# Kernel optimization log

Measured on AMD Instinct MI355X. Metric: run time of the kernel, lower is better.

Reference implementation:

```python
import jax, jax.numpy as jnp
import numpy as np

EPS = 1e-7  # K.epsilon()
NUM_CAPSULE = 32
DIM_CAPSULE = 16
ROUTINGS = 3


def squash(x, axis=-1):
    # NOTE: this repo's squash is pure L2 normalization (no |s|^2/(1+|s|^2) factor)
    s2 = jnp.sum(jnp.square(x), axis=axis, keepdims=True)
    return x / jnp.sqrt(s2 + EPS)


def setup_inputs() -> dict:
    key = jax.random.key(0)
    k1, k2 = jax.random.split(key)
    B, L, D_IN = 32, 2048, 64
    u_vecs = jax.random.normal(k1, (B, L, D_IN), dtype=jnp.float32)
    # glorot-ish scale for the capsule kernel
    W = jax.random.normal(k2, (1, D_IN, NUM_CAPSULE * DIM_CAPSULE), dtype=jnp.float32) * 0.05
    return {"u_vecs": u_vecs, "W": W}


def reference(u_vecs, W):
    B, L, _ = u_vecs.shape
    # K.conv1d with kernel size 1 == pointwise matmul
    u_hat = jnp.einsum('bli,io->blo', u_vecs, W[0])
    u_hat = u_hat.reshape(B, L, NUM_CAPSULE, DIM_CAPSULE)
    u_hat = jnp.transpose(u_hat, (0, 2, 1, 3))  # [B, nc, L, dc]

    b = jnp.zeros((B, NUM_CAPSULE, L), dtype=u_hat.dtype)
    outputs = None
    for i in range(ROUTINGS):
        # softmax over the num_capsule axis (axis=1), per the permute dance in the source
        c = jax.nn.softmax(b, axis=1)  # [B, nc, L]
        outputs = squash(jnp.einsum('bnl,bnld->bnd', c, u_hat))  # [B, nc, dc]
        if i < ROUTINGS - 1:
            b = jnp.einsum('bnd,bnld->bnl', outputs, u_hat)  # overwrite, not accumulate
    return outputs
```

## Files before the change

### kernel.cpp

```cpp
#include <hip/hip_runtime.h>

#define NC 32
#define DC 16
#define LSEQ 2048

__global__ __launch_bounds__(256) void k_sum_u(const float* __restrict__ u,
                                               float* __restrict__ v0p) {
    int b  = blockIdx.x >> 3;
    int l0 = (blockIdx.x & 7) * 256;
    int q  = threadIdx.x & 15;
    int r  = threadIdx.x >> 4;
    const float4* u4 = (const float4*)u;
    float4 acc = {0.f, 0.f, 0.f, 0.f};
#pragma unroll
    for (int j = 0; j < 16; ++j) {
        int l = l0 + r + 16 * j;
        float4 x = u4[(b * LSEQ + l) * 16 + q];
        acc.x += x.x; acc.y += x.y; acc.z += x.z; acc.w += x.w;
    }
    __shared__ float red[16][64];
    red[r][q * 4 + 0] = acc.x;
    red[r][q * 4 + 1] = acc.y;
    red[r][q * 4 + 2] = acc.z;
    red[r][q * 4 + 3] = acc.w;
    __syncthreads();
    if (threadIdx.x < 64) {
        float s = 0.f;
#pragma unroll
        for (int rr = 0; rr < 16; ++rr) s += red[rr][threadIdx.x];
        v0p[blockIdx.x * 64 + threadIdx.x] = s;
    }
}

template <bool BCAST, bool FINAL>
__global__ __launch_bounds__(64) void k_caps(const float* __restrict__ v,
                                             const float* __restrict__ W,
                                             float* __restrict__ wtil,
                                             float* __restrict__ out,
                                             float vscale) {
    int b  = blockIdx.x >> 3;
    int ng = blockIdx.x & 7;
    int t  = threadIdx.x;
    __shared__ float vS[4][72];
    __shared__ float oS[4][16];
    if (BCAST) {
        float s = 0.f;
#pragma unroll
        for (int ch = 0; ch < 8; ++ch) s += v[(b * 8 + ch) * 64 + t];
        s *= vscale;
#pragma unroll
        for (int n4 = 0; n4 < 4; ++n4) vS[n4][t] = s;
    } else {
        int row = t >> 4, col4 = t & 15;
        const float4* v4 = (const float4*)v;
        float4 a = {0.f, 0.f, 0.f, 0.f};
#pragma unroll
        for (int ch = 0; ch < 16; ++ch) {
            float4 x = v4[(b * 16 + ch) * 512 + (ng * 4 + row) * 16 + col4];
            a.x += x.x; a.y += x.y; a.z += x.z; a.w += x.w;
        }
        ((float4*)&vS[row][0])[col4] = a;
    }
    __syncthreads();
    int n4 = t >> 4, d = t & 15;
    int n  = ng * 4 + n4;
    const float* vrow = &vS[n4][0];
    float s = 0.f;
#pragma unroll
    for (int i = 0; i < 64; ++i)
        s = fmaf(vrow[i], W[i * (NC * DC) + n * DC + d], s);
    float s2 = s * s;
#pragma unroll
    for (int off = 8; off >= 1; off >>= 1) s2 += __shfl_xor(s2, off, 16);
    float o = s / sqrtf(s2 + 1e-7f);
    if (FINAL) {
        out[b * (NC * DC) + n * DC + d] = o;
    } else {
        oS[n4][d] = o;
        __syncthreads();
        int i4 = t & 15;
        float4 wv;
        float* wvp = (float*)&wv;
#pragma unroll
        for (int k = 0; k < 4; ++k) {
            int i = i4 * 4 + k;
            float acc = 0.f;
#pragma unroll
            for (int dd = 0; dd < 16; ++dd)
                acc = fmaf(W[i * (NC * DC) + n * DC + dd], oS[n4][dd], acc);
            wvp[k] = acc;
        }
        ((float4*)wtil)[(b * (NC * 64) + n * 64 + i4 * 4) >> 2] = wv;
    }
}

__global__ __launch_bounds__(128) void k_route(const float* __restrict__ u,
                                               const float* __restrict__ wtil,
                                               float* __restrict__ vpart) {
    int b    = blockIdx.x >> 4;
    int ch   = blockIdx.x & 15;
    int l0   = ch * 128;
    int t    = threadIdx.x;
    int w    = t >> 6;
    int lane = t & 63;
    int lr   = lane & 7;
    int lc   = lane >> 3;
    int dr   = lane & 7;
    int nc   = lane >> 3;

    __shared__ float uS[128 * 68];
    __shared__ float wS[32 * 68];
    __shared__ float cS[2 * 2304];
    float4* uS4 = (float4*)uS;
    float4* wS4 = (float4*)wS;
    float*  cw  = cS + w * 2304;
    float4* cw4 = (float4*)cw;

    const float4* ug = (const float4*)(u + (b * LSEQ + l0) * 64);
#pragma unroll
    for (int r = 0; r < 16; ++r) {
        int idx = t + 128 * r;
        uS4[(idx >> 4) * 17 + (idx & 15)] = ug[idx];
    }
    const float4* wg = (const float4*)(wtil + b * (NC * 64));
#pragma unroll
    for (int r = 0; r < 4; ++r) {
        int idx = t + 128 * r;
        wS4[(idx >> 4) * 17 + (idx & 15)] = wg[idx];
    }
    __syncthreads();

    float acc[8][4];
#pragma unroll
    for (int i = 0; i < 8; ++i)
#pragma unroll
        for (int j = 0; j < 4; ++j) acc[i][j] = 0.f;
    int arow = w * 64 + lr;
#pragma unroll 4
    for (int k4 = 0; k4 < 16; ++k4) {
        float4 wf[4];
#pragma unroll
        for (int j = 0; j < 4; ++j) wf[j] = wS4[(lc * 4 + j) * 17 + k4];
#pragma unroll
        for (int i = 0; i < 8; ++i) {
            float4 a = uS4[(arow + 8 * i) * 17 + k4];
#pragma unroll
            for (int j = 0; j < 4; ++j) {
                acc[i][j] = fmaf(a.x, wf[j].x, acc[i][j]);
                acc[i][j] = fmaf(a.y, wf[j].y, acc[i][j]);
                acc[i][j] = fmaf(a.z, wf[j].z, acc[i][j]);
                acc[i][j] = fmaf(a.w, wf[j].w, acc[i][j]);
            }
        }
    }

#pragma unroll
    for (int i = 0; i < 8; ++i) {
        float m = fmaxf(fmaxf(acc[i][0], acc[i][1]), fmaxf(acc[i][2], acc[i][3]));
        m = fmaxf(m, __shfl_xor(m, 8));
        m = fmaxf(m, __shfl_xor(m, 16));
        m = fmaxf(m, __shfl_xor(m, 32));
        float e0 = __expf(acc[i][0] - m), e1 = __expf(acc[i][1] - m);
        float e2 = __expf(acc[i][2] - m), e3 = __expf(acc[i][3] - m);
        float ss = e0 + e1 + e2 + e3;
        ss += __shfl_xor(ss, 8);
        ss += __shfl_xor(ss, 16);
        ss += __shfl_xor(ss, 32);
        float inv = 1.f / ss;
        float4 cvv = {e0 * inv, e1 * inv, e2 * inv, e3 * inv};
        cw4[(lr + 8 * i) * 9 + lc] = cvv;
    }
    __syncthreads();

    float vacc[4][8];
#pragma unroll
    for (int j = 0; j < 4; ++j)
#pragma unroll
        for (int k = 0; k < 8; ++k) vacc[j][k] = 0.f;
#pragma unroll 8
    for (int lrel = 0; lrel < 64; ++lrel) {
        float4 cv = cw4[lrel * 9 + nc];
        const float4* ur = uS4 + (w * 64 + lrel) * 17 + dr * 2;
        float4 u0 = ur[0], u1 = ur[1];
        float* cp = (float*)&cv;
#pragma unroll
        for (int j = 0; j < 4; ++j) {
            float c = cp[j];
            vacc[j][0] = fmaf(c, u0.x, vacc[j][0]);
            vacc[j][1] = fmaf(c, u0.y, vacc[j][1]);
            vacc[j][2] = fmaf(c, u0.z, vacc[j][2]);
            vacc[j][3] = fmaf(c, u0.w, vacc[j][3]);
            vacc[j][4] = fmaf(c, u1.x, vacc[j][4]);
            vacc[j][5] = fmaf(c, u1.y, vacc[j][5]);
            vacc[j][6] = fmaf(c, u1.z, vacc[j][6]);
            vacc[j][7] = fmaf(c, u1.w, vacc[j][7]);
        }
    }

#pragma unroll
    for (int j = 0; j < 4; ++j) {
        float* rp = cw + (nc * 4 + j) * 64 + dr * 8;
        float4 r0 = {vacc[j][0], vacc[j][1], vacc[j][2], vacc[j][3]};
        float4 r1 = {vacc[j][4], vacc[j][5], vacc[j][6], vacc[j][7]};
        ((float4*)rp)[0] = r0;
        ((float4*)rp)[1] = r1;
    }
    __syncthreads();
    float4* cS4 = (float4*)cS;
    float4* vp4 = (float4*)(vpart + blockIdx.x * 2048);
#pragma unroll
    for (int s = 0; s < 4; ++s) {
        int idx4 = t + 128 * s;
        float4 a = cS4[idx4];
        float4 c2 = cS4[576 + idx4];
        float4 o = {a.x + c2.x, a.y + c2.y, a.z + c2.z, a.w + c2.w};
        vp4[idx4] = o;
    }
}

extern "C" void kernel_launch(void* const* d_in, const int* in_sizes, int n_in,
                              void* d_out, int out_size, void* d_ws, size_t ws_size,
                              hipStream_t stream) {
    const float* u = (const float*)d_in[0];
    const float* W = (const float*)d_in[1];
    float* out = (float*)d_out;
    float* ws  = (float*)d_ws;
    float* v0p   = ws;
    float* wt    = ws + 16384;
    float* vpart = ws + 16384 + 65536;

    k_sum_u<<<256, 256, 0, stream>>>(u, v0p);
    k_caps<true, false><<<256, 64, 0, stream>>>(v0p, W, wt, nullptr, 1.0f / 32.0f);
    k_route<<<512, 128, 0, stream>>>(u, wt, vpart);
    k_caps<false, false><<<256, 64, 0, stream>>>(vpart, W, wt, nullptr, 1.0f);
    k_route<<<512, 128, 0, stream>>>(u, wt, vpart);
    k_caps<false, true><<<256, 64, 0, stream>>>(vpart, W, nullptr, out, 1.0f);
}
```

Before: 107.6 us.

## Fuse capsule squash/W-projection into routing kernels via last-block atomic counters

Merges the per-batch capsule computation (v reduction, W projection, squash, and the W·o projection for the next iteration) into the tail of the preceding sum or routing kernel. The last block per batch is detected with an atomic counter and a threadfence, which replaces the separate k_caps launches. This cuts six launches to three plus a memset and regroups block indices so that all chunks of a batch run close together. In exchange, the serial tail work lands on a single 128-thread block per batch and adds atomic and fence overhead.

```diff
diff --git a/kernel.cpp b/kernel.cpp
--- a/kernel.cpp
+++ b/kernel.cpp
@@ -4,125 +4,126 @@
 #define DC 16
 #define LSEQ 2048
 
-__global__ __launch_bounds__(256) void k_sum_u(const float* __restrict__ u,
-                                               float* __restrict__ v0p) {
-    int b  = blockIdx.x >> 3;
-    int l0 = (blockIdx.x & 7) * 256;
-    int q  = threadIdx.x & 15;
-    int r  = threadIdx.x >> 4;
-    const float4* u4 = (const float4*)u;
-    float4 acc = {0.f, 0.f, 0.f, 0.f};
-#pragma unroll
-    for (int j = 0; j < 16; ++j) {
-        int l = l0 + r + 16 * j;
-        float4 x = u4[(b * LSEQ + l) * 16 + q];
-        acc.x += x.x; acc.y += x.y; acc.z += x.z; acc.w += x.w;
-    }
-    __shared__ float red[16][64];
-    red[r][q * 4 + 0] = acc.x;
-    red[r][q * 4 + 1] = acc.y;
-    red[r][q * 4 + 2] = acc.z;
-    red[r][q * 4 + 3] = acc.w;
-    __syncthreads();
-    if (threadIdx.x < 64) {
+
+
+__global__ __launch_bounds__(128) void k_sum_caps0(const float* __restrict__ u,
+                                                   const float* __restrict__ W,
+                                                   float* __restrict__ v0p,
+                                                   float* __restrict__ wtil,
+                                                   int* __restrict__ ctr) {
+    const int rid = blockIdx.x;
+    const int b   = (rid & 7) + ((rid >> 7) << 3);
+    const int j   = (rid >> 3) & 15;
+    const int gb  = b * 16 + j;
+    const int t   = threadIdx.x;
+
+    __shared__ float red[512];
+    __shared__ float vS[64];
+    __shared__ float oS[512];
+    __shared__ int amLast;
+
+    const float4* ug = (const float4*)(u + (b * LSEQ + j * 128) * 64);
+    float4 a = {0.f, 0.f, 0.f, 0.f};
+#pragma unroll
+    for (int r = 0; r < 16; ++r) {
+        float4 x = ug[t + 128 * r];
+        a.x += x.x; a.y += x.y; a.z += x.z; a.w += x.w;
+    }
+    ((float4*)red)[t] = a;
+    __syncthreads();
+    if (t < 64) {
         float s = 0.f;
 #pragma unroll
-        for (int rr = 0; rr < 16; ++rr) s += red[rr][threadIdx.x];
-        v0p[blockIdx.x * 64 + threadIdx.x] = s;
+        for (int g = 0; g < 8; ++g) s += red[t + 64 * g];
+        v0p[gb * 64 + t] = s;
+    }
+    __syncthreads();
+    if (t == 0) {
+        __threadfence();
+        int prev = atomicAdd(&ctr[b * 32 + 0], 1);
+        amLast = (prev == 15);
+    }
+    __syncthreads();
+    if (!amLast) return;
+    __threadfence();
+
+    if (t < 64) {
+        float s = 0.f;
+#pragma unroll
+        for (int ch = 0; ch < 16; ++ch) s += v0p[(b * 16 + ch) * 64 + t];
+        vS[t] = s * (1.f / 32.f);
+    }
+    __syncthreads();
+
+    const int n = t >> 2, d4 = t & 3;
+    const float4* W4 = (const float4*)W;
+    float4 s4 = {0.f, 0.f, 0.f, 0.f};
+#pragma unroll
+    for (int i = 0; i < 64; ++i) {
+        float vi = vS[i];
+        float4 wv = W4[i * 128 + n * 4 + d4];
+        s4.x = fmaf(vi, wv.x, s4.x);
+        s4.y = fmaf(vi, wv.y, s4.y);
+        s4.z = fmaf(vi, wv.z, s4.z);
+        s4.w = fmaf(vi, wv.w, s4.w);
+    }
+    float s2 = s4.x * s4.x + s4.y * s4.y + s4.z * s4.z + s4.w * s4.w;
+    s2 += __shfl_xor(s2, 1);
+    s2 += __shfl_xor(s2, 2);
+    float inv = 1.f / sqrtf(s2 + 1e-7f);
+    float4 o4 = {s4.x * inv, s4.y * inv, s4.z * inv, s4.w * inv};
+    ((float4*)oS)[t] = o4;
+    __syncthreads();
+
+    const float4* oS4 = (const float4*)oS;
+#pragma unroll
+    for (int rep = 0; rep < 16; ++rep) {
+        int idx = t + 128 * rep;
+        int nn = idx >> 6, ii = idx & 63;
+        float acc = 0.f;
+#pragma unroll
+        for (int q = 0; q < 4; ++q) {
+            float4 wv = W4[ii * 128 + nn * 4 + q];
+            float4 ov = oS4[nn * 4 + q];
+            acc += wv.x * ov.x + wv.y * ov.y + wv.z * ov.z + wv.w * ov.w;
+        }
+        wtil[b * (NC * 64) + idx] = acc;
     }
 }
 
-template <bool BCAST, bool FINAL>
-__global__ __launch_bounds__(64) void k_caps(const float* __restrict__ v,
-                                             const float* __restrict__ W,
-                                             float* __restrict__ wtil,
-                                             float* __restrict__ out,
-                                             float vscale) {
-    int b  = blockIdx.x >> 3;
-    int ng = blockIdx.x & 7;
-    int t  = threadIdx.x;
-    __shared__ float vS[4][72];
-    __shared__ float oS[4][16];
-    if (BCAST) {
-        float s = 0.f;
-#pragma unroll
-        for (int ch = 0; ch < 8; ++ch) s += v[(b * 8 + ch) * 64 + t];
-        s *= vscale;
-#pragma unroll
-        for (int n4 = 0; n4 < 4; ++n4) vS[n4][t] = s;
-    } else {
-        int row = t >> 4, col4 = t & 15;
-        const float4* v4 = (const float4*)v;
-        float4 a = {0.f, 0.f, 0.f, 0.f};
-#pragma unroll
-        for (int ch = 0; ch < 16; ++ch) {
-            float4 x = v4[(b * 16 + ch) * 512 + (ng * 4 + row) * 16 + col4];
-            a.x += x.x; a.y += x.y; a.z += x.z; a.w += x.w;
-        }
-        ((float4*)&vS[row][0])[col4] = a;
-    }
-    __syncthreads();
-    int n4 = t >> 4, d = t & 15;
-    int n  = ng * 4 + n4;
-    const float* vrow = &vS[n4][0];
-    float s = 0.f;
-#pragma unroll
-    for (int i = 0; i < 64; ++i)
-        s = fmaf(vrow[i], W[i * (NC * DC) + n * DC + d], s);
-    float s2 = s * s;
-#pragma unroll
-    for (int off = 8; off >= 1; off >>= 1) s2 += __shfl_xor(s2, off, 16);
-    float o = s / sqrtf(s2 + 1e-7f);
-    if (FINAL) {
-        out[b * (NC * DC) + n * DC + d] = o;
-    } else {
-        oS[n4][d] = o;
-        __syncthreads();
-        int i4 = t & 15;
-        float4 wv;
-        float* wvp = (float*)&wv;
-#pragma unroll
-        for (int k = 0; k < 4; ++k) {
-            int i = i4 * 4 + k;
-            float acc = 0.f;
-#pragma unroll
-            for (int dd = 0; dd < 16; ++dd)
-                acc = fmaf(W[i * (NC * DC) + n * DC + dd], oS[n4][dd], acc);
-            wvp[k] = acc;
-        }
-        ((float4*)wtil)[(b * (NC * 64) + n * 64 + i4 * 4) >> 2] = wv;
-    }
-}
-
-__global__ __launch_bounds__(128) void k_route(const float* __restrict__ u,
-                                               const float* __restrict__ wtil,
-                                               float* __restrict__ vpart) {
-    int b    = blockIdx.x >> 4;
-    int ch   = blockIdx.x & 15;
-    int l0   = ch * 128;
-    int t    = threadIdx.x;
-    int w    = t >> 6;
-    int lane = t & 63;
-    int lr   = lane & 7;
-    int lc   = lane >> 3;
-    int dr   = lane & 7;
-    int nc   = lane >> 3;
+template <int PH, bool FINAL>
+__global__ __launch_bounds__(128) void k_route_caps(const float* __restrict__ u,
+                                                    const float* __restrict__ W,
+                                                    const float* __restrict__ wtil_in,
+                                                    float* __restrict__ wtil_out,
+                                                    float* __restrict__ out,
+                                                    float* __restrict__ vpart,
+                                                    int* __restrict__ ctr) {
+    const int rid  = blockIdx.x;
+    const int b    = (rid & 7) + ((rid >> 7) << 3);
+    const int j    = (rid >> 3) & 15;
+    const int gb   = b * 16 + j;
+    const int t    = threadIdx.x;
+    const int w    = t >> 6;
+    const int lane = t & 63;
 
     __shared__ float uS[128 * 68];
     __shared__ float wS[32 * 68];
     __shared__ float cS[2 * 2304];
+    __shared__ int amLast;
     float4* uS4 = (float4*)uS;
     float4* wS4 = (float4*)wS;
+    float4* cS4 = (float4*)cS;
     float*  cw  = cS + w * 2304;
     float4* cw4 = (float4*)cw;
 
-    const float4* ug = (const float4*)(u + (b * LSEQ + l0) * 64);
+    const float4* ug = (const float4*)(u + (b * LSEQ + j * 128) * 64);
 #pragma unroll
     for (int r = 0; r < 16; ++r) {
         int idx = t + 128 * r;
         uS4[(idx >> 4) * 17 + (idx & 15)] = ug[idx];
     }
-    const float4* wg = (const float4*)(wtil + b * (NC * 64));
+    const float4* wg = (const float4*)(wtil_in + b * (NC * 64));
 #pragma unroll
     for (int r = 0; r < 4; ++r) {
         int idx = t + 128 * r;
@@ -130,26 +131,27 @@
     }
     __syncthreads();
 
+    const int lr = lane & 7, lc = lane >> 3;
     float acc[8][4];
 #pragma unroll
     for (int i = 0; i < 8; ++i)
 #pragma unroll
-        for (int j = 0; j < 4; ++j) acc[i][j] = 0.f;
-    int arow = w * 64 + lr;
+        for (int jj = 0; jj < 4; ++jj) acc[i][jj] = 0.f;
+    const int arow = w * 64 + lr;
 #pragma unroll 4
     for (int k4 = 0; k4 < 16; ++k4) {
         float4 wf[4];
 #pragma unroll
-        for (int j = 0; j < 4; ++j) wf[j] = wS4[(lc * 4 + j) * 17 + k4];
+        for (int jj = 0; jj < 4; ++jj) wf[jj] = wS4[(lc * 4 + jj) * 17 + k4];
 #pragma unroll
         for (int i = 0; i < 8; ++i) {
-            float4 a = uS4[(arow + 8 * i) * 17 + k4];
-#pragma unroll
-            for (int j = 0; j < 4; ++j) {
-                acc[i][j] = fmaf(a.x, wf[j].x, acc[i][j]);
-                acc[i][j] = fmaf(a.y, wf[j].y, acc[i][j]);
-                acc[i][j] = fmaf(a.z, wf[j].z, acc[i][j]);
-                acc[i][j] = fmaf(a.w, wf[j].w, acc[i][j]);
+            float4 av = uS4[(arow + 8 * i) * 17 + k4];
+#pragma unroll
+            for (int jj = 0; jj < 4; ++jj) {
+                acc[i][jj] = fmaf(av.x, wf[jj].x, acc[i][jj]);
+                acc[i][jj] = fmaf(av.y, wf[jj].y, acc[i][jj]);
+                acc[i][jj] = fmaf(av.z, wf[jj].z, acc[i][jj]);
+                acc[i][jj] = fmaf(av.w, wf[jj].w, acc[i][jj]);
             }
         }
     }
@@ -172,49 +174,113 @@
     }
     __syncthreads();
 
+    const int dr = lane & 7, ng = lane >> 3;
     float vacc[4][8];
 #pragma unroll
-    for (int j = 0; j < 4; ++j)
-#pragma unroll
-        for (int k = 0; k < 8; ++k) vacc[j][k] = 0.f;
+    for (int jj = 0; jj < 4; ++jj)
+#pragma unroll
+        for (int k = 0; k < 8; ++k) vacc[jj][k] = 0.f;
 #pragma unroll 8
     for (int lrel = 0; lrel < 64; ++lrel) {
-        float4 cv = cw4[lrel * 9 + nc];
+        float4 cv = cw4[lrel * 9 + ng];
         const float4* ur = uS4 + (w * 64 + lrel) * 17 + dr * 2;
         float4 u0 = ur[0], u1 = ur[1];
         float* cp = (float*)&cv;
 #pragma unroll
-        for (int j = 0; j < 4; ++j) {
-            float c = cp[j];
-            vacc[j][0] = fmaf(c, u0.x, vacc[j][0]);
-            vacc[j][1] = fmaf(c, u0.y, vacc[j][1]);
-            vacc[j][2] = fmaf(c, u0.z, vacc[j][2]);
-            vacc[j][3] = fmaf(c, u0.w, vacc[j][3]);
-            vacc[j][4] = fmaf(c, u1.x, vacc[j][4]);
-            vacc[j][5] = fmaf(c, u1.y, vacc[j][5]);
-            vacc[j][6] = fmaf(c, u1.z, vacc[j][6]);
-            vacc[j][7] = fmaf(c, u1.w, vacc[j][7]);
-        }
-    }
-
-#pragma unroll
-    for (int j = 0; j < 4; ++j) {
-        float* rp = cw + (nc * 4 + j) * 64 + dr * 8;
-        float4 r0 = {vacc[j][0], vacc[j][1], vacc[j][2], vacc[j][3]};
-        float4 r1 = {vacc[j][4], vacc[j][5], vacc[j][6], vacc[j][7]};
+        for (int jj = 0; jj < 4; ++jj) {
+            float c = cp[jj];
+            vacc[jj][0] = fmaf(c, u0.x, vacc[jj][0]);
+            vacc[jj][1] = fmaf(c, u0.y, vacc[jj][1]);
+            vacc[jj][2] = fmaf(c, u0.z, vacc[jj][2]);
+            vacc[jj][3] = fmaf(c, u0.w, vacc[jj][3]);
+            vacc[jj][4] = fmaf(c, u1.x, vacc[jj][4]);
+            vacc[jj][5] = fmaf(c, u1.y, vacc[jj][5]);
+            vacc[jj][6] = fmaf(c, u1.z, vacc[jj][6]);
+            vacc[jj][7] = fmaf(c, u1.w, vacc[jj][7]);
+        }
+    }
+#pragma unroll
+    for (int jj = 0; jj < 4; ++jj) {
+        float* rp = cw + (ng * 4 + jj) * 64 + dr * 8;
+        float4 r0 = {vacc[jj][0], vacc[jj][1], vacc[jj][2], vacc[jj][3]};
+        float4 r1 = {vacc[jj][4], vacc[jj][5], vacc[jj][6], vacc[jj][7]};
         ((float4*)rp)[0] = r0;
         ((float4*)rp)[1] = r1;
     }
     __syncthreads();
-    float4* cS4 = (float4*)cS;
-    float4* vp4 = (float4*)(vpart + blockIdx.x * 2048);
-#pragma unroll
-    for (int s = 0; s < 4; ++s) {
-        int idx4 = t + 128 * s;
-        float4 a = cS4[idx4];
-        float4 c2 = cS4[576 + idx4];
-        float4 o = {a.x + c2.x, a.y + c2.y, a.z + c2.z, a.w + c2.w};
+    float4* vp4 = (float4*)(vpart + gb * 2048);
+#pragma unroll
+    for (int sft = 0; sft < 4; ++sft) {
+        int idx4 = t + 128 * sft;
+        float4 x = cS4[idx4];
+        float4 y = cS4[576 + idx4];
+        float4 o = {x.x + y.x, x.y + y.y, x.z + y.z, x.w + y.w};
         vp4[idx4] = o;
+    }
+    __syncthreads();
+
+    if (t == 0) {
+        __threadfence();
+        int prev = atomicAdd(&ctr[b * 32 + PH], 1);
+        amLast = (prev == 15);
+    }
+    __syncthreads();
+    if (!amLast) return;
+    __threadfence();
+
+    const float4* vpb = (const float4*)(vpart + b * 16 * 2048);
+#pragma unroll
+    for (int rep = 0; rep < 4; ++rep) {
+        int idx4 = t + 128 * rep;
+        float4 s = {0.f, 0.f, 0.f, 0.f};
+#pragma unroll
+        for (int ch = 0; ch < 16; ++ch) {
+            float4 x = vpb[ch * 512 + idx4];
+            s.x += x.x; s.y += x.y; s.z += x.z; s.w += x.w;
+        }
+        cS4[(idx4 >> 4) * 17 + (idx4 & 15)] = s;
+    }
+    __syncthreads();
+
+    const int n = t >> 2, d4 = t & 3;
+    const float4* W4 = (const float4*)W;
+    const float* vrow = &cS[n * 68];
+    float4 s4 = {0.f, 0.f, 0.f, 0.f};
+#pragma unroll
+    for (int i = 0; i < 64; ++i) {
+        float vi = vrow[i];
+        float4 wv = W4[i * 128 + n * 4 + d4];
+        s4.x = fmaf(vi, wv.x, s4.x);
+        s4.y = fmaf(vi, wv.y, s4.y);
+        s4.z = fmaf(vi, wv.z, s4.z);
+        s4.w = fmaf(vi, wv.w, s4.w);
+    }
+    float s2 = s4.x * s4.x + s4.y * s4.y + s4.z * s4.z + s4.w * s4.w;
+    s2 += __shfl_xor(s2, 1);
+    s2 += __shfl_xor(s2, 2);
+    float inv = 1.f / sqrtf(s2 + 1e-7f);
+    float4 o4 = {s4.x * inv, s4.y * inv, s4.z * inv, s4.w * inv};
+
+    if (FINAL) {
+        ((float4*)out)[b * 128 + t] = o4;
+        return;
+    }
+    float* oS = cS + 2304;
+    ((float4*)oS)[t] = o4;
+    __syncthreads();
+    const float4* oS4 = (const float4*)oS;
+#pragma unroll
+    for (int rep = 0; rep < 16; ++rep) {
+        int idx = t + 128 * rep;
+        int nn = idx >> 6, ii = idx & 63;
+        float a2 = 0.f;
+#pragma unroll
+        for (int q = 0; q < 4; ++q) {
+            float4 wv = W4[ii * 128 + nn * 4 + q];
+            float4 ov = oS4[nn * 4 + q];
+            a2 += wv.x * ov.x + wv.y * ov.y + wv.z * ov.z + wv.w * ov.w;
+        }
+        wtil_out[b * (NC * 64) + idx] = a2;
     }
 }
 
@@ -225,14 +291,14 @@
     const float* W = (const float*)d_in[1];
     float* out = (float*)d_out;
     float* ws  = (float*)d_ws;
-    float* v0p   = ws;
-    float* wt    = ws + 16384;
-    float* vpart = ws + 16384 + 65536;
-
-    k_sum_u<<<256, 256, 0, stream>>>(u, v0p);
-    k_caps<true, false><<<256, 64, 0, stream>>>(v0p, W, wt, nullptr, 1.0f / 32.0f);
-    k_route<<<512, 128, 0, stream>>>(u, wt, vpart);
-    k_caps<false, false><<<256, 64, 0, stream>>>(vpart, W, wt, nullptr, 1.0f);
-    k_route<<<512, 128, 0, stream>>>(u, wt, vpart);
-    k_caps<false, true><<<256, 64, 0, stream>>>(vpart, W, nullptr, out, 1.0f);
+    int*   ctr   = (int*)ws;
+    float* v0p   = ws + 1024;
+    float* wt    = ws + 1024 + 16384;
+    float* vpart = ws + 1024 + 16384 + 65536;
+
+    hipMemsetAsync(ctr, 0, 32 * 32 * sizeof(int), stream);
+
+    k_sum_caps0<<<512, 128, 0, stream>>>(u, W, v0p, wt, ctr);
+    k_route_caps<1, false><<<512, 128, 0, stream>>>(u, W, wt, wt, nullptr, vpart, ctr);
+    k_route_caps<2, true ><<<512, 128, 0, stream>>>(u, W, wt, nullptr, out, vpart, ctr);
 }
```

After: 155.2 us. 1.44x slower.

## Fuse capsule head into routing kernel and reduce partials with atomics

Applied to the files above, without the earlier changes.

The per-iteration capsule projection and squash step, which computes the W-transformed output vectors, now runs redundantly at the start of every routing block instead of in its own kernel. Partial sums over the sequence are accumulated with global atomicAdd into zeroed workspace instead of being written out and reduced by the next kernel. Routing blocks now use 512 threads over 128 rows, each wave handling 16 rows. Together this cuts the launch count from six kernels to four plus a memset, at the cost of recomputing the head in every block and of atomic contention with nondeterministic summation order.

```diff
diff --git a/kernel.cpp b/kernel.cpp
--- a/kernel.cpp
+++ b/kernel.cpp
@@ -4,158 +4,142 @@
 #define DC 16
 #define LSEQ 2048
 
-__global__ __launch_bounds__(256) void k_sum_u(const float* __restrict__ u,
-                                               float* __restrict__ v0p) {
-    int b  = blockIdx.x >> 3;
-    int l0 = (blockIdx.x & 7) * 256;
-    int q  = threadIdx.x & 15;
-    int r  = threadIdx.x >> 4;
-    const float4* u4 = (const float4*)u;
-    float4 acc = {0.f, 0.f, 0.f, 0.f};
-#pragma unroll
-    for (int j = 0; j < 16; ++j) {
-        int l = l0 + r + 16 * j;
-        float4 x = u4[(b * LSEQ + l) * 16 + q];
-        acc.x += x.x; acc.y += x.y; acc.z += x.z; acc.w += x.w;
+__global__ __launch_bounds__(256) void k_sum(const float* __restrict__ u,
+                                             float* __restrict__ v0) {
+    const int b = blockIdx.x >> 4, j = blockIdx.x & 15;
+    const int t = threadIdx.x;
+    const int q = t & 15, r = t >> 4;
+    const float4* ug = (const float4*)(u + (b * LSEQ + j * 128) * 64);
+    float4 a = {0.f, 0.f, 0.f, 0.f};
+#pragma unroll
+    for (int g = 0; g < 8; ++g) {
+        float4 x = ug[(r + 16 * g) * 16 + q];
+        a.x += x.x; a.y += x.y; a.z += x.z; a.w += x.w;
     }
     __shared__ float red[16][64];
-    red[r][q * 4 + 0] = acc.x;
-    red[r][q * 4 + 1] = acc.y;
-    red[r][q * 4 + 2] = acc.z;
-    red[r][q * 4 + 3] = acc.w;
-    __syncthreads();
-    if (threadIdx.x < 64) {
+    red[r][q * 4 + 0] = a.x;
+    red[r][q * 4 + 1] = a.y;
+    red[r][q * 4 + 2] = a.z;
+    red[r][q * 4 + 3] = a.w;
+    __syncthreads();
+    if (t < 64) {
         float s = 0.f;
 #pragma unroll
-        for (int rr = 0; rr < 16; ++rr) s += red[rr][threadIdx.x];
-        v0p[blockIdx.x * 64 + threadIdx.x] = s;
-    }
-}
-
-template <bool BCAST, bool FINAL>
-__global__ __launch_bounds__(64) void k_caps(const float* __restrict__ v,
-                                             const float* __restrict__ W,
-                                             float* __restrict__ wtil,
-                                             float* __restrict__ out,
-                                             float vscale) {
-    int b  = blockIdx.x >> 3;
-    int ng = blockIdx.x & 7;
-    int t  = threadIdx.x;
-    __shared__ float vS[4][72];
-    __shared__ float oS[4][16];
-    if (BCAST) {
-        float s = 0.f;
-#pragma unroll
-        for (int ch = 0; ch < 8; ++ch) s += v[(b * 8 + ch) * 64 + t];
-        s *= vscale;
-#pragma unroll
-        for (int n4 = 0; n4 < 4; ++n4) vS[n4][t] = s;
+        for (int rr = 0; rr < 16; ++rr) s += red[rr][t];
+        atomicAdd(&v0[b * 64 + t], s);
+    }
+}
+
+template <int ITER0, int FINAL>
+__device__ __forceinline__ void caps_head(int b, int t,
+                                          const float* __restrict__ W,
+                                          const float* __restrict__ vsrc,
+                                          float* wS, float* outg, float* cSc) {
+    float* vf = cSc;
+    float* oS = cSc + 2176;
+    if (ITER0) {
+        if (t < 64) vf[t] = vsrc[b * 64 + t] * (1.f / 32.f);
     } else {
-        int row = t >> 4, col4 = t & 15;
-        const float4* v4 = (const float4*)v;
-        float4 a = {0.f, 0.f, 0.f, 0.f};
-#pragma unroll
-        for (int ch = 0; ch < 16; ++ch) {
-            float4 x = v4[(b * 16 + ch) * 512 + (ng * 4 + row) * 16 + col4];
-            a.x += x.x; a.y += x.y; a.z += x.z; a.w += x.w;
-        }
-        ((float4*)&vS[row][0])[col4] = a;
-    }
-    __syncthreads();
-    int n4 = t >> 4, d = t & 15;
-    int n  = ng * 4 + n4;
-    const float* vrow = &vS[n4][0];
+        float4 s = ((const float4*)(vsrc + b * 2048))[t];
+        ((float4*)vf)[(t >> 4) * 17 + (t & 15)] = s;
+    }
+    __syncthreads();
+    const int n = t >> 4, d = t & 15;
+    const float* vrow = ITER0 ? vf : vf + n * 68;
     float s = 0.f;
 #pragma unroll
     for (int i = 0; i < 64; ++i)
         s = fmaf(vrow[i], W[i * (NC * DC) + n * DC + d], s);
     float s2 = s * s;
-#pragma unroll
-    for (int off = 8; off >= 1; off >>= 1) s2 += __shfl_xor(s2, off, 16);
+    s2 += __shfl_xor(s2, 1);
+    s2 += __shfl_xor(s2, 2);
+    s2 += __shfl_xor(s2, 4);
+    s2 += __shfl_xor(s2, 8);
     float o = s / sqrtf(s2 + 1e-7f);
     if (FINAL) {
-        out[b * (NC * DC) + n * DC + d] = o;
-    } else {
-        oS[n4][d] = o;
-        __syncthreads();
-        int i4 = t & 15;
-        float4 wv;
-        float* wvp = (float*)&wv;
-#pragma unroll
-        for (int k = 0; k < 4; ++k) {
-            int i = i4 * 4 + k;
-            float acc = 0.f;
-#pragma unroll
-            for (int dd = 0; dd < 16; ++dd)
-                acc = fmaf(W[i * (NC * DC) + n * DC + dd], oS[n4][dd], acc);
-            wvp[k] = acc;
-        }
-        ((float4*)wtil)[(b * (NC * 64) + n * 64 + i4 * 4) >> 2] = wv;
-    }
-}
-
-__global__ __launch_bounds__(128) void k_route(const float* __restrict__ u,
-                                               const float* __restrict__ wtil,
-                                               float* __restrict__ vpart) {
-    int b    = blockIdx.x >> 4;
-    int ch   = blockIdx.x & 15;
-    int l0   = ch * 128;
-    int t    = threadIdx.x;
-    int w    = t >> 6;
-    int lane = t & 63;
-    int lr   = lane & 7;
-    int lc   = lane >> 3;
-    int dr   = lane & 7;
-    int nc   = lane >> 3;
-
-    __shared__ float uS[128 * 68];
-    __shared__ float wS[32 * 68];
-    __shared__ float cS[2 * 2304];
+        outg[b * (NC * DC) + t] = o;
+        return;
+    }
+    oS[t] = o;
+    __syncthreads();
+    const float4* o4 = (const float4*)(oS + n * 16);
+    float4 ov0 = o4[0], ov1 = o4[1], ov2 = o4[2], ov3 = o4[3];
+    const int i4 = t & 15;
+    float4 wv;
+    float* wvp = (float*)&wv;
+#pragma unroll
+    for (int k = 0; k < 4; ++k) {
+        const int i = i4 * 4 + k;
+        const float4* wr = (const float4*)(W + i * (NC * DC) + n * DC);
+        float4 w0 = wr[0], w1 = wr[1], w2 = wr[2], w3 = wr[3];
+        float acc = w0.x * ov0.x + w0.y * ov0.y + w0.z * ov0.z + w0.w * ov0.w;
+        acc += w1.x * ov1.x + w1.y * ov1.y + w1.z * ov1.z + w1.w * ov1.w;
+        acc += w2.x * ov2.x + w2.y * ov2.y + w2.z * ov2.z + w2.w * ov2.w;
+        acc += w3.x * ov3.x + w3.y * ov3.y + w3.z * ov3.z + w3.w * ov3.w;
+        wvp[k] = acc;
+    }
+    ((float4*)wS)[n * 17 + i4] = wv;
+}
+
+template <int ITER0>
+__global__ __launch_bounds__(512, 4) void k_route(const float* __restrict__ u,
+                                                  const float* __restrict__ W,
+                                                  const float* __restrict__ vin,
+                                                  float* __restrict__ vout) {
+    const int rid = blockIdx.x;
+    const int b = rid >> 4, j = rid & 15;
+    const int t = threadIdx.x;
+    const int w = t >> 6, lane = t & 63;
+
+    __shared__ float smem[15488];
+    float* uS = smem;
+    float* wS = smem + 8704;
+    float* cS = smem + 10880;
     float4* uS4 = (float4*)uS;
     float4* wS4 = (float4*)wS;
-    float*  cw  = cS + w * 2304;
-    float4* cw4 = (float4*)cw;
-
-    const float4* ug = (const float4*)(u + (b * LSEQ + l0) * 64);
-#pragma unroll
-    for (int r = 0; r < 16; ++r) {
-        int idx = t + 128 * r;
-        uS4[(idx >> 4) * 17 + (idx & 15)] = ug[idx];
-    }
-    const float4* wg = (const float4*)(wtil + b * (NC * 64));
+    float4* c4  = (float4*)cS;
+
+    const float4* ug = (const float4*)(u + (b * LSEQ + j * 128) * 64);
+    float4 ur[4];
+#pragma unroll
+    for (int r = 0; r < 4; ++r) ur[r] = ug[t + 512 * r];
+
+    caps_head<ITER0, 0>(b, t, W, vin, wS, nullptr, cS);
+
 #pragma unroll
     for (int r = 0; r < 4; ++r) {
-        int idx = t + 128 * r;
-        wS4[(idx >> 4) * 17 + (idx & 15)] = wg[idx];
-    }
-    __syncthreads();
-
-    float acc[8][4];
-#pragma unroll
-    for (int i = 0; i < 8; ++i)
-#pragma unroll
-        for (int j = 0; j < 4; ++j) acc[i][j] = 0.f;
-    int arow = w * 64 + lr;
+        int idx = t + 512 * r;
+        uS4[(idx >> 4) * 17 + (idx & 15)] = ur[r];
+    }
+    __syncthreads();
+
+    const int lw = w * 16;
+    const int lr = lane & 7, lc = lane >> 3;
+    float acc[2][4];
+#pragma unroll
+    for (int i = 0; i < 2; ++i)
+#pragma unroll
+        for (int jj = 0; jj < 4; ++jj) acc[i][jj] = 0.f;
 #pragma unroll 4
     for (int k4 = 0; k4 < 16; ++k4) {
         float4 wf[4];
 #pragma unroll
-        for (int j = 0; j < 4; ++j) wf[j] = wS4[(lc * 4 + j) * 17 + k4];
-#pragma unroll
-        for (int i = 0; i < 8; ++i) {
-            float4 a = uS4[(arow + 8 * i) * 17 + k4];
-#pragma unroll
-            for (int j = 0; j < 4; ++j) {
-                acc[i][j] = fmaf(a.x, wf[j].x, acc[i][j]);
-                acc[i][j] = fmaf(a.y, wf[j].y, acc[i][j]);
-                acc[i][j] = fmaf(a.z, wf[j].z, acc[i][j]);
-                acc[i][j] = fmaf(a.w, wf[j].w, acc[i][j]);
+        for (int jj = 0; jj < 4; ++jj) wf[jj] = wS4[(lc * 4 + jj) * 17 + k4];
+#pragma unroll
+        for (int i = 0; i < 2; ++i) {
+            float4 av = uS4[(lw + lr + 8 * i) * 17 + k4];
+#pragma unroll
+            for (int jj = 0; jj < 4; ++jj) {
+                acc[i][jj] = fmaf(av.x, wf[jj].x, acc[i][jj]);
+                acc[i][jj] = fmaf(av.y, wf[jj].y, acc[i][jj]);
+                acc[i][jj] = fmaf(av.z, wf[jj].z, acc[i][jj]);
+                acc[i][jj] = fmaf(av.w, wf[jj].w, acc[i][jj]);
             }
         }
     }
 
 #pragma unroll
-    for (int i = 0; i < 8; ++i) {
+    for (int i = 0; i < 2; ++i) {
         float m = fmaxf(fmaxf(acc[i][0], acc[i][1]), fmaxf(acc[i][2], acc[i][3]));
         m = fmaxf(m, __shfl_xor(m, 8));
         m = fmaxf(m, __shfl_xor(m, 16));
@@ -167,55 +151,85 @@
         ss += __shfl_xor(ss, 16);
         ss += __shfl_xor(ss, 32);
         float inv = 1.f / ss;
-        float4 cvv = {e0 * inv, e1 * inv, e2 * inv, e3 * inv};
-        cw4[(lr + 8 * i) * 9 + lc] = cvv;
-    }
-    __syncthreads();
-
+        float4 cv = {e0 * inv, e1 * inv, e2 * inv, e3 * inv};
+        c4[(lw + lr + 8 * i) * 9 + lc] = cv;
+    }
+    __syncthreads();
+
+    const int dr = lane & 7, ng = lane >> 3;
     float vacc[4][8];
 #pragma unroll
-    for (int j = 0; j < 4; ++j)
-#pragma unroll
-        for (int k = 0; k < 8; ++k) vacc[j][k] = 0.f;
-#pragma unroll 8
-    for (int lrel = 0; lrel < 64; ++lrel) {
-        float4 cv = cw4[lrel * 9 + nc];
-        const float4* ur = uS4 + (w * 64 + lrel) * 17 + dr * 2;
-        float4 u0 = ur[0], u1 = ur[1];
-        float* cp = (float*)&cv;
-#pragma unroll
-        for (int j = 0; j < 4; ++j) {
-            float c = cp[j];
-            vacc[j][0] = fmaf(c, u0.x, vacc[j][0]);
-            vacc[j][1] = fmaf(c, u0.y, vacc[j][1]);
-            vacc[j][2] = fmaf(c, u0.z, vacc[j][2]);
-            vacc[j][3] = fmaf(c, u0.w, vacc[j][3]);
-            vacc[j][4] = fmaf(c, u1.x, vacc[j][4]);
-            vacc[j][5] = fmaf(c, u1.y, vacc[j][5]);
-            vacc[j][6] = fmaf(c, u1.z, vacc[j][6]);
-            vacc[j][7] = fmaf(c, u1.w, vacc[j][7]);
-        }
-    }
-
-#pragma unroll
-    for (int j = 0; j < 4; ++j) {
-        float* rp = cw + (nc * 4 + j) * 64 + dr * 8;
-        float4 r0 = {vacc[j][0], vacc[j][1], vacc[j][2], vacc[j][3]};
-        float4 r1 = {vacc[j][4], vacc[j][5], vacc[j][6], vacc[j][7]};
-        ((float4*)rp)[0] = r0;
-        ((float4*)rp)[1] = r1;
-    }
-    __syncthreads();
-    float4* cS4 = (float4*)cS;
-    float4* vp4 = (float4*)(vpart + blockIdx.x * 2048);
-#pragma unroll
-    for (int s = 0; s < 4; ++s) {
-        int idx4 = t + 128 * s;
-        float4 a = cS4[idx4];
-        float4 c2 = cS4[576 + idx4];
-        float4 o = {a.x + c2.x, a.y + c2.y, a.z + c2.z, a.w + c2.w};
-        vp4[idx4] = o;
-    }
+    for (int jj = 0; jj < 4; ++jj)
+#pragma unroll
+        for (int k = 0; k < 8; ++k) vacc[jj][k] = 0.f;
+#pragma unroll
+    for (int lrel = 0; lrel < 16; ++lrel) {
+        const int row = lw + lrel;
+        float4 cv = c4[row * 9 + ng];
+        const float4* up = uS4 + row * 17 + dr * 2;
+        float4 u0 = up[0], u1 = up[1];
+        const float* cp = (const float*)&cv;
+#pragma unroll
+        for (int jj = 0; jj < 4; ++jj) {
+            float c = cp[jj];
+            vacc[jj][0] = fmaf(c, u0.x, vacc[jj][0]);
+            vacc[jj][1] = fmaf(c, u0.y, vacc[jj][1]);
+            vacc[jj][2] = fmaf(c, u0.z, vacc[jj][2]);
+            vacc[jj][3] = fmaf(c, u0.w, vacc[jj][3]);
+            vacc[jj][4] = fmaf(c, u1.x, vacc[jj][4]);
+            vacc[jj][5] = fmaf(c, u1.y, vacc[jj][5]);
+            vacc[jj][6] = fmaf(c, u1.z, vacc[jj][6]);
+            vacc[jj][7] = fmaf(c, u1.w, vacc[jj][7]);
+        }
+    }
+    __syncthreads();
+
+    float* red = smem;
+    const int p = w >> 1;
+    if (w & 1) {
+#pragma unroll
+        for (int jj = 0; jj < 4; ++jj) {
+            float4* rp = (float4*)(red + p * 2048 + (ng * 4 + jj) * 64 + dr * 8);
+            float4 r0 = {vacc[jj][0], vacc[jj][1], vacc[jj][2], vacc[jj][3]};
+            float4 r1 = {vacc[jj][4], vacc[jj][5], vacc[jj][6], vacc[jj][7]};
+            rp[0] = r0;
+            rp[1] = r1;
+        }
+    }
+    __syncthreads();
+    if (!(w & 1)) {
+#pragma unroll
+        for (int jj = 0; jj < 4; ++jj) {
+            float4* rp = (float4*)(red + p * 2048 + (ng * 4 + jj) * 64 + dr * 8);
+            float4 r0 = rp[0], r1 = rp[1];
+            r0.x += vacc[jj][0]; r0.y += vacc[jj][1];
+            r0.z += vacc[jj][2]; r0.w += vacc[jj][3];
+            r1.x += vacc[jj][4]; r1.y += vacc[jj][5];
+            r1.z += vacc[jj][6]; r1.w += vacc[jj][7];
+            rp[0] = r0;
+            rp[1] = r1;
+        }
+    }
+    __syncthreads();
+    {
+        float4* red4 = (float4*)red;
+        float4 a0 = red4[t], a1 = red4[512 + t];
+        float4 a2 = red4[1024 + t], a3 = red4[1536 + t];
+        float4 o = {a0.x + a1.x + a2.x + a3.x, a0.y + a1.y + a2.y + a3.y,
+                    a0.z + a1.z + a2.z + a3.z, a0.w + a1.w + a2.w + a3.w};
+        float* vp = vout + b * 2048 + t * 4;
+        atomicAdd(vp + 0, o.x);
+        atomicAdd(vp + 1, o.y);
+        atomicAdd(vp + 2, o.z);
+        atomicAdd(vp + 3, o.w);
+    }
+}
+
+__global__ __launch_bounds__(512) void k_caps_final(const float* __restrict__ W,
+                                                    const float* __restrict__ vin,
+                                                    float* __restrict__ out) {
+    __shared__ float cSf[2688];
+    caps_head<0, 1>((int)blockIdx.x, (int)threadIdx.x, W, vin, nullptr, out, cSf);
 }
 
 extern "C" void kernel_launch(void* const* d_in, const int* in_sizes, int n_in,
@@ -225,14 +239,14 @@
     const float* W = (const float*)d_in[1];
     float* out = (float*)d_out;
     float* ws  = (float*)d_ws;
-    float* v0p   = ws;
-    float* wt    = ws + 16384;
-    float* vpart = ws + 16384 + 65536;
-
-    k_sum_u<<<256, 256, 0, stream>>>(u, v0p);
-    k_caps<true, false><<<256, 64, 0, stream>>>(v0p, W, wt, nullptr, 1.0f / 32.0f);
-    k_route<<<512, 128, 0, stream>>>(u, wt, vpart);
-    k_caps<false, false><<<256, 64, 0, stream>>>(vpart, W, wt, nullptr, 1.0f);
-    k_route<<<512, 128, 0, stream>>>(u, wt, vpart);
-    k_caps<false, true><<<256, 64, 0, stream>>>(vpart, W, nullptr, out, 1.0f);
-}
+    float* v0 = ws;
+    float* v1 = ws + 2048;
+    float* v2 = ws + 2048 + 65536;
+
+    hipMemsetAsync(ws, 0, (2048 + 65536 + 65536) * sizeof(float), stream);
+
+    k_sum<<<512, 256, 0, stream>>>(u, v0);
+    k_route<1><<<512, 512, 0, stream>>>(u, W, v0, v1);
+    k_route<0><<<512, 512, 0, stream>>>(u, W, v1, v2);
+    k_caps_final<<<32, 512, 0, stream>>>(W, v2, out);
+}
```

Result: slower. 139.8 us (+29.9%).

## Use 256 threads per routing block with four waves and tree reduction

Applied to the files above, without the earlier changes.

The routing kernel goes from two wavefronts to four per block. Each wave now handles 32 sequence rows instead of 64, so each thread holds half the logits accumulators. The softmax coefficient buffer becomes one shared array indexed by row, and the per-wave partial capsule sums are reduced through the reused u tile in two stages. This is meant to raise parallelism and latency hiding per block, at the cost of extra barriers and shared-memory reduction traffic.

```diff
diff --git a/kernel.cpp b/kernel.cpp
--- a/kernel.cpp
+++ b/kernel.cpp
@@ -94,7 +94,7 @@
     }
 }
 
-__global__ __launch_bounds__(128) void k_route(const float* __restrict__ u,
+__global__ __launch_bounds__(256) void k_route(const float* __restrict__ u,
                                                const float* __restrict__ wtil,
                                                float* __restrict__ vpart) {
     int b    = blockIdx.x >> 4;
@@ -106,56 +106,55 @@
     int lr   = lane & 7;
     int lc   = lane >> 3;
     int dr   = lane & 7;
-    int nc   = lane >> 3;
+    int ng   = lane >> 3;
 
     __shared__ float uS[128 * 68];
     __shared__ float wS[32 * 68];
-    __shared__ float cS[2 * 2304];
+    __shared__ float cS[128 * 36];
     float4* uS4 = (float4*)uS;
     float4* wS4 = (float4*)wS;
-    float*  cw  = cS + w * 2304;
-    float4* cw4 = (float4*)cw;
+    float4* c4  = (float4*)cS;
 
     const float4* ug = (const float4*)(u + (b * LSEQ + l0) * 64);
 #pragma unroll
-    for (int r = 0; r < 16; ++r) {
-        int idx = t + 128 * r;
+    for (int r = 0; r < 8; ++r) {
+        int idx = t + 256 * r;
         uS4[(idx >> 4) * 17 + (idx & 15)] = ug[idx];
     }
     const float4* wg = (const float4*)(wtil + b * (NC * 64));
 #pragma unroll
-    for (int r = 0; r < 4; ++r) {
-        int idx = t + 128 * r;
+    for (int r = 0; r < 2; ++r) {
+        int idx = t + 256 * r;
         wS4[(idx >> 4) * 17 + (idx & 15)] = wg[idx];
     }
     __syncthreads();
 
-    float acc[8][4];
-#pragma unroll
-    for (int i = 0; i < 8; ++i)
-#pragma unroll
-        for (int j = 0; j < 4; ++j) acc[i][j] = 0.f;
-    int arow = w * 64 + lr;
+    float acc[4][4];
+#pragma unroll
+    for (int i = 0; i < 4; ++i)
+#pragma unroll
+        for (int jj = 0; jj < 4; ++jj) acc[i][jj] = 0.f;
+    int arow = w * 32 + lr;
 #pragma unroll 4
     for (int k4 = 0; k4 < 16; ++k4) {
         float4 wf[4];
 #pragma unroll
-        for (int j = 0; j < 4; ++j) wf[j] = wS4[(lc * 4 + j) * 17 + k4];
-#pragma unroll
-        for (int i = 0; i < 8; ++i) {
+        for (int jj = 0; jj < 4; ++jj) wf[jj] = wS4[(lc + 8 * jj) * 17 + k4];
+#pragma unroll
+        for (int i = 0; i < 4; ++i) {
             float4 a = uS4[(arow + 8 * i) * 17 + k4];
 #pragma unroll
-            for (int j = 0; j < 4; ++j) {
-                acc[i][j] = fmaf(a.x, wf[j].x, acc[i][j]);
-                acc[i][j] = fmaf(a.y, wf[j].y, acc[i][j]);
-                acc[i][j] = fmaf(a.z, wf[j].z, acc[i][j]);
-                acc[i][j] = fmaf(a.w, wf[j].w, acc[i][j]);
+            for (int jj = 0; jj < 4; ++jj) {
+                acc[i][jj] = fmaf(a.x, wf[jj].x, acc[i][jj]);
+                acc[i][jj] = fmaf(a.y, wf[jj].y, acc[i][jj]);
+                acc[i][jj] = fmaf(a.z, wf[jj].z, acc[i][jj]);
+                acc[i][jj] = fmaf(a.w, wf[jj].w, acc[i][jj]);
             }
         }
     }
 
 #pragma unroll
-    for (int i = 0; i < 8; ++i) {
+    for (int i = 0; i < 4; ++i) {
         float m = fmaxf(fmaxf(acc[i][0], acc[i][1]), fmaxf(acc[i][2], acc[i][3]));
         m = fmaxf(m, __shfl_xor(m, 8));
         m = fmaxf(m, __shfl_xor(m, 16));
@@ -168,52 +167,72 @@
         ss += __shfl_xor(ss, 32);
         float inv = 1.f / ss;
         float4 cvv = {e0 * inv, e1 * inv, e2 * inv, e3 * inv};
-        cw4[(lr + 8 * i) * 9 + lc] = cvv;
+        c4[(arow + 8 * i) * 9 + lc] = cvv;
     }
     __syncthreads();
 
     float vacc[4][8];
 #pragma unroll
-    for (int j = 0; j < 4; ++j)
-#pragma unroll
-        for (int k = 0; k < 8; ++k) vacc[j][k] = 0.f;
+    for (int jj = 0; jj < 4; ++jj)
+#pragma unroll
+        for (int k = 0; k < 8; ++k) vacc[jj][k] = 0.f;
 #pragma unroll 8
-    for (int lrel = 0; lrel < 64; ++lrel) {
-        float4 cv = cw4[lrel * 9 + nc];
-        const float4* ur = uS4 + (w * 64 + lrel) * 17 + dr * 2;
+    for (int lrel = 0; lrel < 32; ++lrel) {
+        int row = w * 32 + lrel;
+        float4 cv = c4[row * 9 + ng];
+        const float4* ur = uS4 + row * 17 + dr * 2;
         float4 u0 = ur[0], u1 = ur[1];
         float* cp = (float*)&cv;
 #pragma unroll
-        for (int j = 0; j < 4; ++j) {
-            float c = cp[j];
-            vacc[j][0] = fmaf(c, u0.x, vacc[j][0]);
-            vacc[j][1] = fmaf(c, u0.y, vacc[j][1]);
-            vacc[j][2] = fmaf(c, u0.z, vacc[j][2]);
-            vacc[j][3] = fmaf(c, u0.w, vacc[j][3]);
-            vacc[j][4] = fmaf(c, u1.x, vacc[j][4]);
-            vacc[j][5] = fmaf(c, u1.y, vacc[j][5]);
-            vacc[j][6] = fmaf(c, u1.z, vacc[j][6]);
-            vacc[j][7] = fmaf(c, u1.w, vacc[j][7]);
-        }
-    }
-
-#pragma unroll
-    for (int j = 0; j < 4; ++j) {
-        float* rp = cw + (nc * 4 + j) * 64 + dr * 8;
-        float4 r0 = {vacc[j][0], vacc[j][1], vacc[j][2], vacc[j][3]};
-        float4 r1 = {vacc[j][4], vacc[j][5], vacc[j][6], vacc[j][7]};
-        ((float4*)rp)[0] = r0;
-        ((float4*)rp)[1] = r1;
-    }
-    __syncthreads();
-    float4* cS4 = (float4*)cS;
-    float4* vp4 = (float4*)(vpart + blockIdx.x * 2048);
-#pragma unroll
-    for (int s = 0; s < 4; ++s) {
-        int idx4 = t + 128 * s;
-        float4 a = cS4[idx4];
-        float4 c2 = cS4[576 + idx4];
-        float4 o = {a.x + c2.x, a.y + c2.y, a.z + c2.z, a.w + c2.w};
+        for (int jj = 0; jj < 4; ++jj) {
+            float c = cp[jj];
+            vacc[jj][0] = fmaf(c, u0.x, vacc[jj][0]);
+            vacc[jj][1] = fmaf(c, u0.y, vacc[jj][1]);
+            vacc[jj][2] = fmaf(c, u0.z, vacc[jj][2]);
+            vacc[jj][3] = fmaf(c, u0.w, vacc[jj][3]);
+            vacc[jj][4] = fmaf(c, u1.x, vacc[jj][4]);
+            vacc[jj][5] = fmaf(c, u1.y, vacc[jj][5]);
+            vacc[jj][6] = fmaf(c, u1.z, vacc[jj][6]);
+            vacc[jj][7] = fmaf(c, u1.w, vacc[jj][7]);
+        }
+    }
+    __syncthreads();
+
+    float* red   = uS;
+    float* rbase = red + (w >> 1) * 2048;
+    if (w & 1) {
+#pragma unroll
+        for (int jj = 0; jj < 4; ++jj) {
+            float4* rp = (float4*)(rbase + (ng + 8 * jj) * 64 + dr * 8);
+            float4 r0 = {vacc[jj][0], vacc[jj][1], vacc[jj][2], vacc[jj][3]};
+            float4 r1 = {vacc[jj][4], vacc[jj][5], vacc[jj][6], vacc[jj][7]};
+            rp[0] = r0;
+            rp[1] = r1;
+        }
+    }
+    __syncthreads();
+    if (!(w & 1)) {
+#pragma unroll
+        for (int jj = 0; jj < 4; ++jj) {
+            float4* rp = (float4*)(rbase + (ng + 8 * jj) * 64 + dr * 8);
+            float4 r0 = rp[0], r1 = rp[1];
+            r0.x += vacc[jj][0]; r0.y += vacc[jj][1];
+            r0.z += vacc[jj][2]; r0.w += vacc[jj][3];
+            r1.x += vacc[jj][4]; r1.y += vacc[jj][5];
+            r1.z += vacc[jj][6]; r1.w += vacc[jj][7];
+            rp[0] = r0;
+            rp[1] = r1;
+        }
+    }
+    __syncthreads();
+    float4* red4 = (float4*)red;
+    float4* vp4  = (float4*)(vpart + blockIdx.x * 2048);
+#pragma unroll
+    for (int s = 0; s < 2; ++s) {
+        int idx4 = t + 256 * s;
+        float4 a  = red4[idx4];
+        float4 c2 = red4[512 + idx4];
+        float4 o  = {a.x + c2.x, a.y + c2.y, a.z + c2.z, a.w + c2.w};
         vp4[idx4] = o;
     }
 }
@@ -231,8 +250,8 @@
 
     k_sum_u<<<256, 256, 0, stream>>>(u, v0p);
     k_caps<true, false><<<256, 64, 0, stream>>>(v0p, W, wt, nullptr, 1.0f / 32.0f);
-    k_route<<<512, 128, 0, stream>>>(u, wt, vpart);
+    k_route<<<512, 256, 0, stream>>>(u, wt, vpart);
     k_caps<false, false><<<256, 64, 0, stream>>>(vpart, W, wt, nullptr, 1.0f);
-    k_route<<<512, 128, 0, stream>>>(u, wt, vpart);
+    k_route<<<512, 256, 0, stream>>>(u, wt, vpart);
     k_caps<false, true><<<256, 64, 0, stream>>>(vpart, W, nullptr, out, 1.0f);
 }
```

After: 100.0 us (median of 2 runs). 1.08x faster.
